# Kernel tuning notes

Measured on AMD Instinct MI355X. Metric: run time of the kernel, lower is better.

Reference implementation:

```python
import jax, jax.numpy as jnp
import numpy as np
from math import factorial

P = 3          # polynomial order
D_I = 4096     # sketch output dim per order
C = 512        # input channels
B, H, W = 8, 28, 28
GAMMA = 1e-4


def setup_inputs() -> dict:
    key = jax.random.key(0)
    k1, k2, k3 = jax.random.split(key, 3)
    x = jax.random.normal(k1, (B, H, W, C), dtype=jnp.float32)
    # AlphaInitializer: alpha_i = sqrt(exp(-2g) * (2g)^i / i!)
    gam2 = np.full(P + 1, 2.0 * GAMMA)
    numer = np.power(gam2, np.arange(P + 1))
    denom = np.array([factorial(i) for i in range(P + 1)], dtype=np.float64)
    alpha = jnp.asarray(np.sqrt(np.exp(-gam2) * numer / denom), dtype=jnp.float32)
    # count-sketch hash indices and sign bits, one pair per order t in [0, p)
    h_idx = jax.random.randint(k2, (P, C), 0, D_I)
    s_bits = jax.random.randint(k3, (P, C), 0, 2).astype(jnp.int32)
    return {"x": x, "alpha": alpha, "h_idx": h_idx, "s_bits": s_bits}


def reference(x, alpha, h_idx, s_bits):
    Bs, Hs, Ws, Ch = x.shape
    p = h_idx.shape[0]
    d_i = D_I
    signs = (2 * s_bits - 1).astype(x.dtype)          # (p, C) in {-1,+1}
    x_flat = x.reshape(-1, Ch)                        # (B*H*W, C)

    def count_sketch(h, s):
        # scatter-add channels into d_i buckets: equivalent to x_flat @ S
        return jnp.zeros((x_flat.shape[0], d_i), x.dtype).at[:, h].add(x_flat * s)

    sk = jax.vmap(count_sketch)(h_idx, signs)         # (p, N, d_i)
    xs = jnp.transpose(sk, (1, 0, 2)).reshape(Bs, Hs * Ws, p, d_i)

    xf = jnp.fft.fft(xs.astype(jnp.complex64), axis=-1)
    cp = jnp.cumprod(xf, axis=-2)[:, :, 1:, :]        # orders 2..p
    xi = jnp.real(jnp.fft.ifft(cp, axis=-1)).mean(axis=1)   # (B, p-1, d_i)

    x_p = xi * alpha[2:].reshape(1, p - 1, 1)
    zeroth = alpha[0] * jnp.ones((Bs, 1), x.dtype)
    first = alpha[1] * x.mean(axis=(1, 2))            # (B, C)
    phi = jnp.concatenate([zeroth, first, x_p.reshape(Bs, -1)], axis=-1)
    phi = jnp.sign(phi) * jnp.sqrt(jnp.abs(phi) + 1e-12)    # signed sqrt
    return phi / jnp.linalg.norm(phi, axis=-1, keepdims=True)
```

## Files before the change

### kernel.cpp

```cpp
#include <hip/hip_runtime.h>

#define BATCH 8
#define NPOS 784
#define CH 512
#define DI 4096
#define PPC 8
#define CHUNKS (NPOS / PPC)
#define PHI_LEN 8705
#define S_FLOATS (BATCH * 2 * 2049 * 2)
#define PHI_OFF S_FLOATS

__device__ __forceinline__ float2 cmul(float2 a, float2 b) {
  return make_float2(a.x * b.x - a.y * b.y, a.x * b.y + a.y * b.x);
}
__device__ __forceinline__ float2 f2add(float2 a, float2 b) {
  return make_float2(a.x + b.x, a.y + b.y);
}
__device__ __forceinline__ float2 f2sub(float2 a, float2 b) {
  return make_float2(a.x - b.x, a.y - b.y);
}

__device__ __forceinline__ void dft4(float2& a, float2& b, float2& c, float2& d) {
  float t0x = a.x + c.x, t0y = a.y + c.y;
  float t1x = a.x - c.x, t1y = a.y - c.y;
  float t2x = b.x + d.x, t2y = b.y + d.y;
  float t3x = b.x - d.x, t3y = b.y - d.y;
  a = make_float2(t0x + t2x, t0y + t2y);
  c = make_float2(t0x - t2x, t0y - t2y);
  b = make_float2(t1x + t3y, t1y - t3x);
  d = make_float2(t1x - t3y, t1y + t3x);
}

__device__ __forceinline__ void dft8(float2 v[8]) {
  float2 e0 = v[0], e1 = v[2], e2 = v[4], e3 = v[6];
  dft4(e0, e1, e2, e3);
  float2 o0 = v[1], o1 = v[3], o2 = v[5], o3 = v[7];
  dft4(o0, o1, o2, o3);
  const float r = 0.70710678118654752f;
  o1 = make_float2(r * (o1.x + o1.y), r * (o1.y - o1.x));
  o2 = make_float2(o2.y, -o2.x);
  o3 = make_float2(r * (o3.y - o3.x), -r * (o3.x + o3.y));
  v[0] = f2add(e0, o0); v[4] = f2sub(e0, o0);
  v[1] = f2add(e1, o1); v[5] = f2sub(e1, o1);
  v[2] = f2add(e2, o2); v[6] = f2sub(e2, o2);
  v[3] = f2add(e3, o3); v[7] = f2sub(e3, o3);
}

__device__ __forceinline__ void twiddle8(float2 v[8], float2 w) {
  float2 w2 = cmul(w, w);
  float2 w3 = cmul(w2, w);
  float2 w4 = cmul(w2, w2);
  v[1] = cmul(v[1], w);
  v[2] = cmul(v[2], w2);
  v[3] = cmul(v[3], w3);
  v[4] = cmul(v[4], w4);
  v[5] = cmul(v[5], cmul(w4, w));
  v[6] = cmul(v[6], cmul(w4, w2));
  v[7] = cmul(v[7], cmul(w4, w3));
}

__device__ __forceinline__ void fstage0(float2* Z, int t) {
  const int base = t << 3;
  const int mask0 = (t >> 1) & 15;
  float2 v[8];
  #pragma unroll
  for (int u = 0; u < 8; ++u) v[u] = Z[(base + u) ^ mask0];
  dft8(v);
  #pragma unroll
  for (int k = 0; k < 8; ++k) Z[(base + k) ^ mask0] = v[k];
}
__device__ __forceinline__ void fstage1(float2* Z, int t) {
  const int base = ((t >> 3) << 6) + (t & 7);
  const int g4 = (t >> 3) << 2;
  float sv_, cv_;
  __sincosf(-9.8174770424681038e-2f * (float)(t & 7), &sv_, &cv_);
  const float2 w1b = make_float2(cv_, sv_);
  float2 v[8];
  #pragma unroll
  for (int u = 0; u < 8; ++u)
    v[u] = Z[(base + (u << 3)) ^ ((g4 + (u >> 1)) & 15)];
  twiddle8(v, w1b);
  dft8(v);
  #pragma unroll
  for (int k = 0; k < 8; ++k)
    Z[(base + (k << 3)) ^ ((g4 + (k >> 1)) & 15)] = v[k];
}
__device__ __forceinline__ void fstage2(float2* Z, int t) {
  const int base = ((t >> 6) << 9) + (t & 63);
  const int jh = (t & 63) >> 4;
  float sv_, cv_;
  __sincosf(-1.2271846303085130e-2f * (float)(t & 63), &sv_, &cv_);
  const float2 w2b = make_float2(cv_, sv_);
  float2 v[8];
  #pragma unroll
  for (int u = 0; u < 8; ++u)
    v[u] = Z[(base + (u << 6)) ^ (((u << 2) + jh) & 15)];
  twiddle8(v, w2b);
  dft8(v);
  #pragma unroll
  for (int k = 0; k < 8; ++k)
    Z[(base + (k << 6)) ^ (((k << 2) + jh) & 15)] = v[k];
}
__device__ __forceinline__ void fstage3(float2* Z, int t) {
  const int mask3 = (t >> 4) & 15;
  float sv_, cv_;
  __sincosf(-1.5339807878856412e-3f * (float)t, &sv_, &cv_);
  const float2 w3b = make_float2(cv_, sv_);
  float2 v[8];
  #pragma unroll
  for (int u = 0; u < 8; ++u) v[u] = Z[(t + (u << 9)) ^ mask3];
  twiddle8(v, w3b);
  dft8(v);
  #pragma unroll
  for (int k = 0; k < 8; ++k) Z[(t + (k << 9)) ^ mask3] = v[k];
}

template <int MODE>
__device__ __forceinline__ void product_phase(
    float2* Z, int t, float2 carry[4], float2 acc2[4], float2 acc3[4],
    float& carryx, float& acc2x, float& acc3x) {
  const int mask3 = (t >> 4) & 15;
  #pragma unroll
  for (int jj = 0; jj < 4; ++jj) {
    const int k = t + (jj << 9);
    const int ak = k ^ mask3;
    const int m = (DI - k) & (DI - 1);
    const int am = m ^ ((m >> 4) & 15);
    float2 Zk = Z[ak], Zm = Z[am];
    Z[ak] = make_float2(0.f, 0.f);
    Z[am] = make_float2(0.f, 0.f);
    float2 E = make_float2(0.5f * (Zk.x + Zm.x), 0.5f * (Zk.y - Zm.y));
    float2 O = make_float2(0.5f * (Zk.y + Zm.y), -0.5f * (Zk.x - Zm.x));
    if (MODE == 0) {
      float2 P = cmul(E, O);
      carry[jj] = P;
      acc2[jj].x += P.x; acc2[jj].y += P.y;
    } else if (MODE == 1) {
      float2 P3 = cmul(carry[jj], E);
      acc3[jj].x += P3.x; acc3[jj].y += P3.y;
      carry[jj] = O;
    } else {
      float2 P = cmul(carry[jj], E);
      acc2[jj].x += P.x; acc2[jj].y += P.y;
      float2 P3 = cmul(P, O);
      acc3[jj].x += P3.x; acc3[jj].y += P3.y;
    }
  }
  if (t == 0) {
    float2 Zq = Z[2048];
    Z[2048] = make_float2(0.f, 0.f);
    if (MODE == 0) { carryx = Zq.x * Zq.y; acc2x += carryx; }
    else if (MODE == 1) { acc3x += carryx * Zq.x; carryx = Zq.y; }
    else { float tt = carryx * Zq.x; acc2x += tt; acc3x += tt * Zq.y; }
  }
}

__global__ __launch_bounds__(512) void cbp_stage1(
    const float* __restrict__ x, const float* __restrict__ alpha,
    const int* __restrict__ h_idx, const int* __restrict__ s_bits,
    float* __restrict__ ws) {
  __shared__ float2 ZA[DI];
  __shared__ float2 ZB[DI];
  float* ZAf = (float*)ZA;
  float* ZBf = (float*)ZB;
  const int t = threadIdx.x;
  const int bb = blockIdx.x / CHUNKS;
  const int ch = blockIdx.x % CHUNKS;

  auto mapq = [](int h, int s) {
    int r = ((h & 7) << 9) | (((h >> 3) & 7) << 6) | (((h >> 6) & 7) << 3) |
            (h >> 9);
    return (r ^ ((r >> 4) & 15)) | ((s ^ 1) << 31);
  };
  auto sgn = [](float v, int p) {
    return __int_as_float(__float_as_int(v) ^ ((unsigned)p & 0x80000000u));
  };
  const int q0 = mapq(h_idx[t], s_bits[t]);
  const int q1 = mapq(h_idx[CH + t], s_bits[CH + t]);
  const int q2 = mapq(h_idx[2 * CH + t], s_bits[2 * CH + t]);

  float2 acc2[4], acc3[4], carryA[4], carryB[4];
  #pragma unroll
  for (int j = 0; j < 4; ++j) {
    acc2[j] = make_float2(0.f, 0.f);
    acc3[j] = make_float2(0.f, 0.f);
  }
  float acc2x = 0.f, acc3x = 0.f, carryxA = 0.f, carryxB = 0.f;
  float xs = 0.f;

  #pragma unroll
  for (int q = 0; q < 8; ++q) {
    ZA[t + (q << 9)] = make_float2(0.f, 0.f);
    ZB[t + (q << 9)] = make_float2(0.f, 0.f);
  }
  __syncthreads();

  for (int ip = 0; ip < PPC / 4; ++ip) {
    const int n0 = bb * NPOS + ch * PPC + ip * 4;
    const float a0 = x[(size_t)n0 * CH + t];
    const float a1 = x[(size_t)(n0 + 1) * CH + t];
    const float b0 = x[(size_t)(n0 + 2) * CH + t];
    const float b1 = x[(size_t)(n0 + 3) * CH + t];
    xs += a0 + a1 + b0 + b1;

    atomicAdd(&ZAf[2 * (q0 & 0xFFF)], sgn(a0, q0));
    atomicAdd(&ZAf[2 * (q1 & 0xFFF) + 1], sgn(a0, q1));
    atomicAdd(&ZBf[2 * (q0 & 0xFFF)], sgn(b0, q0));
    atomicAdd(&ZBf[2 * (q1 & 0xFFF) + 1], sgn(b0, q1));
    __syncthreads();
    fstage0(ZA, t); fstage0(ZB, t); __syncthreads();
    fstage1(ZA, t); fstage1(ZB, t); __syncthreads();
    fstage2(ZA, t); fstage2(ZB, t); __syncthreads();
    fstage3(ZA, t); fstage3(ZB, t); __syncthreads();
    product_phase<0>(ZA, t, carryA, acc2, acc3, carryxA, acc2x, acc3x);
    product_phase<0>(ZB, t, carryB, acc2, acc3, carryxB, acc2x, acc3x);
    __syncthreads();

    atomicAdd(&ZAf[2 * (q2 & 0xFFF)], sgn(a0, q2));
    atomicAdd(&ZAf[2 * (q0 & 0xFFF) + 1], sgn(a1, q0));
    atomicAdd(&ZBf[2 * (q2 & 0xFFF)], sgn(b0, q2));
    atomicAdd(&ZBf[2 * (q0 & 0xFFF) + 1], sgn(b1, q0));
    __syncthreads();
    fstage0(ZA, t); fstage0(ZB, t); __syncthreads();
    fstage1(ZA, t); fstage1(ZB, t); __syncthreads();
    fstage2(ZA, t); fstage2(ZB, t); __syncthreads();
    fstage3(ZA, t); fstage3(ZB, t); __syncthreads();
    product_phase<1>(ZA, t, carryA, acc2, acc3, carryxA, acc2x, acc3x);
    product_phase<1>(ZB, t, carryB, acc2, acc3, carryxB, acc2x, acc3x);
    __syncthreads();

    atomicAdd(&ZAf[2 * (q1 & 0xFFF)], sgn(a1, q1));
    atomicAdd(&ZAf[2 * (q2 & 0xFFF) + 1], sgn(a1, q2));
    atomicAdd(&ZBf[2 * (q1 & 0xFFF)], sgn(b1, q1));
    atomicAdd(&ZBf[2 * (q2 & 0xFFF) + 1], sgn(b1, q2));
    __syncthreads();
    fstage0(ZA, t); fstage0(ZB, t); __syncthreads();
    fstage1(ZA, t); fstage1(ZB, t); __syncthreads();
    fstage2(ZA, t); fstage2(ZB, t); __syncthreads();
    fstage3(ZA, t); fstage3(ZB, t); __syncthreads();
    product_phase<2>(ZA, t, carryA, acc2, acc3, carryxA, acc2x, acc3x);
    product_phase<2>(ZB, t, carryB, acc2, acc3, carryxB, acc2x, acc3x);
    __syncthreads();
  }

  float* S = ws;
  #pragma unroll
  for (int jj = 0; jj < 4; ++jj) {
    const int k = t + (jj << 9);
    float* p2p = S + ((size_t)(bb * 2 + 0) * 2049 + k) * 2;
    atomicAdd(p2p, acc2[jj].x);
    atomicAdd(p2p + 1, acc2[jj].y);
    float* p3p = S + ((size_t)(bb * 2 + 1) * 2049 + k) * 2;
    atomicAdd(p3p, acc3[jj].x);
    atomicAdd(p3p + 1, acc3[jj].y);
  }
  if (t == 0) {
    atomicAdd(S + ((size_t)(bb * 2 + 0) * 2049 + 2048) * 2, acc2x);
    atomicAdd(S + ((size_t)(bb * 2 + 1) * 2049 + 2048) * 2, acc3x);
  }

  const float sc1 = alpha[1] * (1.0f / (float)NPOS);
  float* phi = ws + PHI_OFF;
  atomicAdd(&phi[(size_t)bb * PHI_LEN + 1 + t], xs * sc1);
}

__device__ inline void fft4096_r2(float2* Z, const float2* W, int tid) {
  for (int s = 1; s <= 12; ++s) {
    __syncthreads();
    const int half = 1 << (s - 1);
    const int tsh = 12 - s;
    #pragma unroll
    for (int q = 0; q < 8; ++q) {
      int bidx = tid + q * 256;
      int j = bidx & (half - 1);
      int i1 = ((bidx >> (s - 1)) << s) + j;
      int i2 = i1 + half;
      float2 w = W[j << tsh];
      float2 u = Z[i1];
      float2 v = Z[i2];
      float2 t = cmul(w, v);
      Z[i1] = make_float2(u.x + t.x, u.y + t.y);
      Z[i2] = make_float2(u.x - t.x, u.y - t.y);
    }
  }
  __syncthreads();
}

__global__ __launch_bounds__(256) void cbp_stage2(
    const float* __restrict__ ws_in, const float* __restrict__ alpha,
    float* __restrict__ ws_phi) {
  __shared__ float2 Z[DI];
  __shared__ float2 W[DI / 2];
  const int tid = threadIdx.x;

  for (int r = tid; r < DI / 2; r += 256) {
    float ang = 1.5339807878856412e-3f * (float)r;
    float sv, cv;
    sincosf(ang, &sv, &cv);
    W[r] = make_float2(cv, sv);
  }

  const int b = blockIdx.x >> 1;
  const int t = blockIdx.x & 1;
  const float* Sp = ws_in + (size_t)(b * 2 + t) * 2049 * 2;

  for (int k = tid; k <= 2048; k += 256) {
    float re = Sp[k * 2];
    float im = Sp[k * 2 + 1];
    Z[__brev((unsigned)k) >> 20] = make_float2(re, im);
    if (k > 0 && k < 2048) {
      Z[__brev((unsigned)(DI - k)) >> 20] = make_float2(re, -im);
    }
  }
  fft4096_r2(Z, W, tid);

  const float scale = alpha[2 + t] / ((float)DI * (float)NPOS);
  float* out = ws_phi + (size_t)b * PHI_LEN + 513 + t * DI;
  for (int d = tid; d < DI; d += 256) out[d] = Z[d].x * scale;
}

__global__ __launch_bounds__(256) void cbp_stage3(
    const float* __restrict__ ws_phi, const float* __restrict__ alpha,
    float* __restrict__ out) {
  __shared__ float red[4];
  const int b = blockIdx.x;
  const int tid = threadIdx.x;
  const float* pr = ws_phi + (size_t)b * PHI_LEN;
  const float a0 = alpha[0];

  float w[35];
  float ssum = 0.f;
  #pragma unroll
  for (int j = 0; j < 35; ++j) {
    const int idx = tid + j * 256;
    float wv = 0.f;
    if (idx < PHI_LEN) {
      float v = (idx == 0) ? a0 : pr[idx];
      float sq = sqrtf(fabsf(v) + 1e-12f);
      wv = (v > 0.f) ? sq : ((v < 0.f) ? -sq : 0.f);
    }
    w[j] = wv;
    ssum += wv * wv;
  }
  for (int off = 32; off > 0; off >>= 1) ssum += __shfl_down(ssum, off);
  if ((tid & 63) == 0) red[tid >> 6] = ssum;
  __syncthreads();
  const float tot = red[0] + red[1] + red[2] + red[3];
  const float inv = 1.0f / sqrtf(tot);

  #pragma unroll
  for (int j = 0; j < 35; ++j) {
    const int idx = tid + j * 256;
    if (idx < PHI_LEN) out[(size_t)b * PHI_LEN + idx] = w[j] * inv;
  }
}

extern "C" void kernel_launch(void* const* d_in, const int* in_sizes, int n_in,
                              void* d_out, int out_size, void* d_ws,
                              size_t ws_size, hipStream_t stream) {
  const float* x = (const float*)d_in[0];
  const float* alpha = (const float*)d_in[1];
  const int* h_idx = (const int*)d_in[2];
  const int* s_bits = (const int*)d_in[3];
  float* out = (float*)d_out;
  float* ws = (float*)d_ws;

  const size_t zero_bytes = (size_t)(S_FLOATS + BATCH * PHI_LEN) * sizeof(float);
  hipMemsetAsync(d_ws, 0, zero_bytes, stream);

  cbp_stage1<<<dim3(BATCH * CHUNKS), dim3(512), 0, stream>>>(x, alpha, h_idx,
                                                             s_bits, ws);
  cbp_stage2<<<dim3(BATCH * 2), dim3(256), 0, stream>>>(ws, alpha,
                                                        ws + PHI_OFF);
  cbp_stage3<<<dim3(BATCH), dim3(256), 0, stream>>>(ws + PHI_OFF, alpha, out);
}
```

Before: 241.7 us.

## Halve stage1 block to 256 threads with one FFT buffer and fused final stage

Reworks the sketch/FFT kernel to use 256 threads with a single 4096-point shared buffer. Each thread now handles two channels, loaded as a float2, and two butterfly groups per stage. The last radix-8 FFT stage is fused with the pointwise spectral product by pairing each thread's outputs with the mirror-index thread (512-t), which removes one barrier and one shared-memory round trip per FFT. Shared memory per block is halved to raise occupancy (launch_bounds 256,4), at the cost of more registers per thread and half as many positions processed concurrently per block.

```diff
diff --git a/kernel.cpp b/kernel.cpp
--- a/kernel.cpp
+++ b/kernel.cpp
@@ -59,113 +59,146 @@
   v[7] = cmul(v[7], cmul(w4, w3));
 }
 
-__device__ __forceinline__ void fstage0(float2* Z, int t) {
+__device__ __forceinline__ void s0pair(float2* Z, int t) {
   const int base = t << 3;
-  const int mask0 = (t >> 1) & 15;
-  float2 v[8];
-  #pragma unroll
-  for (int u = 0; u < 8; ++u) v[u] = Z[(base + u) ^ mask0];
-  dft8(v);
-  #pragma unroll
-  for (int k = 0; k < 8; ++k) Z[(base + k) ^ mask0] = v[k];
-}
-__device__ __forceinline__ void fstage1(float2* Z, int t) {
+  const int m0 = (t >> 1) & 15;
+  float2 a[8], b[8];
+  #pragma unroll
+  for (int u = 0; u < 8; ++u) a[u] = Z[(base + u) ^ m0];
+  #pragma unroll
+  for (int u = 0; u < 8; ++u) b[u] = Z[(2048 + base + u) ^ m0];
+  dft8(a);
+  #pragma unroll
+  for (int k = 0; k < 8; ++k) Z[(base + k) ^ m0] = a[k];
+  dft8(b);
+  #pragma unroll
+  for (int k = 0; k < 8; ++k) Z[(2048 + base + k) ^ m0] = b[k];
+}
+__device__ __forceinline__ void s1pair(float2* Z, int t) {
   const int base = ((t >> 3) << 6) + (t & 7);
   const int g4 = (t >> 3) << 2;
   float sv_, cv_;
   __sincosf(-9.8174770424681038e-2f * (float)(t & 7), &sv_, &cv_);
-  const float2 w1b = make_float2(cv_, sv_);
-  float2 v[8];
+  const float2 w = make_float2(cv_, sv_);
+  float2 a[8], b[8];
   #pragma unroll
   for (int u = 0; u < 8; ++u)
-    v[u] = Z[(base + (u << 3)) ^ ((g4 + (u >> 1)) & 15)];
-  twiddle8(v, w1b);
-  dft8(v);
+    a[u] = Z[(base + (u << 3)) ^ ((g4 + (u >> 1)) & 15)];
+  #pragma unroll
+  for (int u = 0; u < 8; ++u)
+    b[u] = Z[(2048 + base + (u << 3)) ^ ((g4 + (u >> 1)) & 15)];
+  twiddle8(a, w); dft8(a);
   #pragma unroll
   for (int k = 0; k < 8; ++k)
-    Z[(base + (k << 3)) ^ ((g4 + (k >> 1)) & 15)] = v[k];
-}
-__device__ __forceinline__ void fstage2(float2* Z, int t) {
+    Z[(base + (k << 3)) ^ ((g4 + (k >> 1)) & 15)] = a[k];
+  twiddle8(b, w); dft8(b);
+  #pragma unroll
+  for (int k = 0; k < 8; ++k)
+    Z[(2048 + base + (k << 3)) ^ ((g4 + (k >> 1)) & 15)] = b[k];
+}
+__device__ __forceinline__ void s2pair(float2* Z, int t) {
   const int base = ((t >> 6) << 9) + (t & 63);
   const int jh = (t & 63) >> 4;
   float sv_, cv_;
   __sincosf(-1.2271846303085130e-2f * (float)(t & 63), &sv_, &cv_);
-  const float2 w2b = make_float2(cv_, sv_);
-  float2 v[8];
+  const float2 w = make_float2(cv_, sv_);
+  float2 a[8], b[8];
   #pragma unroll
   for (int u = 0; u < 8; ++u)
-    v[u] = Z[(base + (u << 6)) ^ (((u << 2) + jh) & 15)];
-  twiddle8(v, w2b);
-  dft8(v);
+    a[u] = Z[(base + (u << 6)) ^ (((u << 2) + jh) & 15)];
+  #pragma unroll
+  for (int u = 0; u < 8; ++u)
+    b[u] = Z[(2048 + base + (u << 6)) ^ (((u << 2) + jh) & 15)];
+  twiddle8(a, w); dft8(a);
   #pragma unroll
   for (int k = 0; k < 8; ++k)
-    Z[(base + (k << 6)) ^ (((k << 2) + jh) & 15)] = v[k];
-}
-__device__ __forceinline__ void fstage3(float2* Z, int t) {
-  const int mask3 = (t >> 4) & 15;
+    Z[(base + (k << 6)) ^ (((k << 2) + jh) & 15)] = a[k];
+  twiddle8(b, w); dft8(b);
+  #pragma unroll
+  for (int k = 0; k < 8; ++k)
+    Z[(2048 + base + (k << 6)) ^ (((k << 2) + jh) & 15)] = b[k];
+}
+
+template <int MODE>
+__device__ __forceinline__ void prodpair(float2 Zk, float2 Zm, float2& carry,
+                                         float2& acc2, float2& acc3) {
+  float2 E = make_float2(0.5f * (Zk.x + Zm.x), 0.5f * (Zk.y - Zm.y));
+  float2 O = make_float2(0.5f * (Zk.y + Zm.y), -0.5f * (Zk.x - Zm.x));
+  if (MODE == 0) {
+    float2 P = cmul(E, O);
+    carry = P;
+    acc2.x += P.x; acc2.y += P.y;
+  } else if (MODE == 1) {
+    float2 P3 = cmul(carry, E);
+    acc3.x += P3.x; acc3.y += P3.y;
+    carry = O;
+  } else {
+    float2 P = cmul(carry, E);
+    acc2.x += P.x; acc2.y += P.y;
+    float2 P3 = cmul(P, O);
+    acc3.x += P3.x; acc3.y += P3.y;
+  }
+}
+template <int MODE>
+__device__ __forceinline__ void nyq(float2 Zq, float& carryx, float& acc2x,
+                                    float& acc3x) {
+  if (MODE == 0) { carryx = Zq.x * Zq.y; acc2x += carryx; }
+  else if (MODE == 1) { acc3x += carryx * Zq.x; carryx = Zq.y; }
+  else { float tt = carryx * Zq.x; acc2x += tt; acc3x += tt * Zq.y; }
+}
+
+template <int MODE>
+__device__ __forceinline__ void s3prod(float2* Z, int t, int bB,
+                                       float2 carry[8], float2 acc2[8],
+                                       float2 acc3[8], float& carryx,
+                                       float& acc2x, float& acc3x) {
+  const int mA = (t >> 4) & 15;
+  const int mB = (bB >> 4) & 15;
+  float2 a[8], b[8];
+  #pragma unroll
+  for (int u = 0; u < 8; ++u) a[u] = Z[(t + (u << 9)) ^ mA];
+  #pragma unroll
+  for (int u = 0; u < 8; ++u) b[u] = Z[(bB + (u << 9)) ^ mB];
+  #pragma unroll
+  for (int u = 0; u < 8; ++u) Z[(t + (u << 9)) ^ mA] = make_float2(0.f, 0.f);
+  #pragma unroll
+  for (int u = 0; u < 8; ++u) Z[(bB + (u << 9)) ^ mB] = make_float2(0.f, 0.f);
   float sv_, cv_;
   __sincosf(-1.5339807878856412e-3f * (float)t, &sv_, &cv_);
-  const float2 w3b = make_float2(cv_, sv_);
-  float2 v[8];
-  #pragma unroll
-  for (int u = 0; u < 8; ++u) v[u] = Z[(t + (u << 9)) ^ mask3];
-  twiddle8(v, w3b);
-  dft8(v);
-  #pragma unroll
-  for (int k = 0; k < 8; ++k) Z[(t + (k << 9)) ^ mask3] = v[k];
-}
-
-template <int MODE>
-__device__ __forceinline__ void product_phase(
-    float2* Z, int t, float2 carry[4], float2 acc2[4], float2 acc3[4],
-    float& carryx, float& acc2x, float& acc3x) {
-  const int mask3 = (t >> 4) & 15;
-  #pragma unroll
-  for (int jj = 0; jj < 4; ++jj) {
-    const int k = t + (jj << 9);
-    const int ak = k ^ mask3;
-    const int m = (DI - k) & (DI - 1);
-    const int am = m ^ ((m >> 4) & 15);
-    float2 Zk = Z[ak], Zm = Z[am];
-    Z[ak] = make_float2(0.f, 0.f);
-    Z[am] = make_float2(0.f, 0.f);
-    float2 E = make_float2(0.5f * (Zk.x + Zm.x), 0.5f * (Zk.y - Zm.y));
-    float2 O = make_float2(0.5f * (Zk.y + Zm.y), -0.5f * (Zk.x - Zm.x));
-    if (MODE == 0) {
-      float2 P = cmul(E, O);
-      carry[jj] = P;
-      acc2[jj].x += P.x; acc2[jj].y += P.y;
-    } else if (MODE == 1) {
-      float2 P3 = cmul(carry[jj], E);
-      acc3[jj].x += P3.x; acc3[jj].y += P3.y;
-      carry[jj] = O;
-    } else {
-      float2 P = cmul(carry[jj], E);
-      acc2[jj].x += P.x; acc2[jj].y += P.y;
-      float2 P3 = cmul(P, O);
-      acc3[jj].x += P3.x; acc3[jj].y += P3.y;
-    }
-  }
-  if (t == 0) {
-    float2 Zq = Z[2048];
-    Z[2048] = make_float2(0.f, 0.f);
-    if (MODE == 0) { carryx = Zq.x * Zq.y; acc2x += carryx; }
-    else if (MODE == 1) { acc3x += carryx * Zq.x; carryx = Zq.y; }
-    else { float tt = carryx * Zq.x; acc2x += tt; acc3x += tt * Zq.y; }
-  }
-}
-
-__global__ __launch_bounds__(512) void cbp_stage1(
+  twiddle8(a, make_float2(cv_, sv_));
+  dft8(a);
+  __sincosf(-1.5339807878856412e-3f * (float)bB, &sv_, &cv_);
+  twiddle8(b, make_float2(cv_, sv_));
+  dft8(b);
+  if (t != 0) {
+    #pragma unroll
+    for (int u = 0; u < 4; ++u)
+      prodpair<MODE>(a[u], b[7 - u], carry[u], acc2[u], acc3[u]);
+    #pragma unroll
+    for (int u = 0; u < 4; ++u)
+      prodpair<MODE>(b[u], a[7 - u], carry[4 + u], acc2[4 + u], acc3[4 + u]);
+  } else {
+    prodpair<MODE>(a[0], a[0], carry[0], acc2[0], acc3[0]);
+    prodpair<MODE>(a[1], a[7], carry[1], acc2[1], acc3[1]);
+    prodpair<MODE>(a[2], a[6], carry[2], acc2[2], acc3[2]);
+    prodpair<MODE>(a[3], a[5], carry[3], acc2[3], acc3[3]);
+    #pragma unroll
+    for (int u = 0; u < 4; ++u)
+      prodpair<MODE>(b[u], b[7 - u], carry[4 + u], acc2[4 + u], acc3[4 + u]);
+    nyq<MODE>(a[4], carryx, acc2x, acc3x);
+  }
+}
+
+__global__ __launch_bounds__(256, 4) void cbp_stage1(
     const float* __restrict__ x, const float* __restrict__ alpha,
     const int* __restrict__ h_idx, const int* __restrict__ s_bits,
     float* __restrict__ ws) {
-  __shared__ float2 ZA[DI];
-  __shared__ float2 ZB[DI];
-  float* ZAf = (float*)ZA;
-  float* ZBf = (float*)ZB;
+  __shared__ float2 Z[DI];
+  float* Zf = (float*)Z;
   const int t = threadIdx.x;
   const int bb = blockIdx.x / CHUNKS;
   const int ch = blockIdx.x % CHUNKS;
+  const int bB = (t == 0) ? 256 : (512 - t);
 
   auto mapq = [](int h, int s) {
     int r = ((h & 7) << 9) | (((h >> 3) & 7) << 6) | (((h >> 6) & 7) << 3) |
@@ -175,78 +208,72 @@
   auto sgn = [](float v, int p) {
     return __int_as_float(__float_as_int(v) ^ ((unsigned)p & 0x80000000u));
   };
-  const int q0 = mapq(h_idx[t], s_bits[t]);
-  const int q1 = mapq(h_idx[CH + t], s_bits[CH + t]);
-  const int q2 = mapq(h_idx[2 * CH + t], s_bits[2 * CH + t]);
-
-  float2 acc2[4], acc3[4], carryA[4], carryB[4];
-  #pragma unroll
-  for (int j = 0; j < 4; ++j) {
+  const int c0 = t * 2, c1 = c0 + 1;
+  const int q0a = mapq(h_idx[c0], s_bits[c0]);
+  const int q0b = mapq(h_idx[c1], s_bits[c1]);
+  const int q1a = mapq(h_idx[CH + c0], s_bits[CH + c0]);
+  const int q1b = mapq(h_idx[CH + c1], s_bits[CH + c1]);
+  const int q2a = mapq(h_idx[2 * CH + c0], s_bits[2 * CH + c0]);
+  const int q2b = mapq(h_idx[2 * CH + c1], s_bits[2 * CH + c1]);
+
+  float2 acc2[8], acc3[8], carry[8];
+  #pragma unroll
+  for (int j = 0; j < 8; ++j) {
     acc2[j] = make_float2(0.f, 0.f);
     acc3[j] = make_float2(0.f, 0.f);
   }
-  float acc2x = 0.f, acc3x = 0.f, carryxA = 0.f, carryxB = 0.f;
-  float xs = 0.f;
-
-  #pragma unroll
-  for (int q = 0; q < 8; ++q) {
-    ZA[t + (q << 9)] = make_float2(0.f, 0.f);
-    ZB[t + (q << 9)] = make_float2(0.f, 0.f);
-  }
+  float acc2x = 0.f, acc3x = 0.f, carryx = 0.f;
+  float xsa = 0.f, xsb = 0.f;
+
+  #pragma unroll
+  for (int q = 0; q < 16; ++q) Z[t + (q << 8)] = make_float2(0.f, 0.f);
   __syncthreads();
 
-  for (int ip = 0; ip < PPC / 4; ++ip) {
-    const int n0 = bb * NPOS + ch * PPC + ip * 4;
-    const float a0 = x[(size_t)n0 * CH + t];
-    const float a1 = x[(size_t)(n0 + 1) * CH + t];
-    const float b0 = x[(size_t)(n0 + 2) * CH + t];
-    const float b1 = x[(size_t)(n0 + 3) * CH + t];
-    xs += a0 + a1 + b0 + b1;
-
-    atomicAdd(&ZAf[2 * (q0 & 0xFFF)], sgn(a0, q0));
-    atomicAdd(&ZAf[2 * (q1 & 0xFFF) + 1], sgn(a0, q1));
-    atomicAdd(&ZBf[2 * (q0 & 0xFFF)], sgn(b0, q0));
-    atomicAdd(&ZBf[2 * (q1 & 0xFFF) + 1], sgn(b0, q1));
-    __syncthreads();
-    fstage0(ZA, t); fstage0(ZB, t); __syncthreads();
-    fstage1(ZA, t); fstage1(ZB, t); __syncthreads();
-    fstage2(ZA, t); fstage2(ZB, t); __syncthreads();
-    fstage3(ZA, t); fstage3(ZB, t); __syncthreads();
-    product_phase<0>(ZA, t, carryA, acc2, acc3, carryxA, acc2x, acc3x);
-    product_phase<0>(ZB, t, carryB, acc2, acc3, carryxB, acc2x, acc3x);
-    __syncthreads();
-
-    atomicAdd(&ZAf[2 * (q2 & 0xFFF)], sgn(a0, q2));
-    atomicAdd(&ZAf[2 * (q0 & 0xFFF) + 1], sgn(a1, q0));
-    atomicAdd(&ZBf[2 * (q2 & 0xFFF)], sgn(b0, q2));
-    atomicAdd(&ZBf[2 * (q0 & 0xFFF) + 1], sgn(b1, q0));
-    __syncthreads();
-    fstage0(ZA, t); fstage0(ZB, t); __syncthreads();
-    fstage1(ZA, t); fstage1(ZB, t); __syncthreads();
-    fstage2(ZA, t); fstage2(ZB, t); __syncthreads();
-    fstage3(ZA, t); fstage3(ZB, t); __syncthreads();
-    product_phase<1>(ZA, t, carryA, acc2, acc3, carryxA, acc2x, acc3x);
-    product_phase<1>(ZB, t, carryB, acc2, acc3, carryxB, acc2x, acc3x);
-    __syncthreads();
-
-    atomicAdd(&ZAf[2 * (q1 & 0xFFF)], sgn(a1, q1));
-    atomicAdd(&ZAf[2 * (q2 & 0xFFF) + 1], sgn(a1, q2));
-    atomicAdd(&ZBf[2 * (q1 & 0xFFF)], sgn(b1, q1));
-    atomicAdd(&ZBf[2 * (q2 & 0xFFF) + 1], sgn(b1, q2));
-    __syncthreads();
-    fstage0(ZA, t); fstage0(ZB, t); __syncthreads();
-    fstage1(ZA, t); fstage1(ZB, t); __syncthreads();
-    fstage2(ZA, t); fstage2(ZB, t); __syncthreads();
-    fstage3(ZA, t); fstage3(ZB, t); __syncthreads();
-    product_phase<2>(ZA, t, carryA, acc2, acc3, carryxA, acc2x, acc3x);
-    product_phase<2>(ZB, t, carryB, acc2, acc3, carryxB, acc2x, acc3x);
+  for (int ip = 0; ip < PPC / 2; ++ip) {
+    const int n0 = bb * NPOS + ch * PPC + ip * 2;
+    const float2 xv0 = *(const float2*)(x + (size_t)n0 * CH + c0);
+    const float2 xv1 = *(const float2*)(x + (size_t)(n0 + 1) * CH + c0);
+    xsa += xv0.x + xv1.x;
+    xsb += xv0.y + xv1.y;
+
+    atomicAdd(&Zf[2 * (q0a & 0xFFF)], sgn(xv0.x, q0a));
+    atomicAdd(&Zf[2 * (q0b & 0xFFF)], sgn(xv0.y, q0b));
+    atomicAdd(&Zf[2 * (q1a & 0xFFF) + 1], sgn(xv0.x, q1a));
+    atomicAdd(&Zf[2 * (q1b & 0xFFF) + 1], sgn(xv0.y, q1b));
+    __syncthreads();
+    s0pair(Z, t); __syncthreads();
+    s1pair(Z, t); __syncthreads();
+    s2pair(Z, t); __syncthreads();
+    s3prod<0>(Z, t, bB, carry, acc2, acc3, carryx, acc2x, acc3x);
+    __syncthreads();
+
+    atomicAdd(&Zf[2 * (q2a & 0xFFF)], sgn(xv0.x, q2a));
+    atomicAdd(&Zf[2 * (q2b & 0xFFF)], sgn(xv0.y, q2b));
+    atomicAdd(&Zf[2 * (q0a & 0xFFF) + 1], sgn(xv1.x, q0a));
+    atomicAdd(&Zf[2 * (q0b & 0xFFF) + 1], sgn(xv1.y, q0b));
+    __syncthreads();
+    s0pair(Z, t); __syncthreads();
+    s1pair(Z, t); __syncthreads();
+    s2pair(Z, t); __syncthreads();
+    s3prod<1>(Z, t, bB, carry, acc2, acc3, carryx, acc2x, acc3x);
+    __syncthreads();
+
+    atomicAdd(&Zf[2 * (q1a & 0xFFF)], sgn(xv1.x, q1a));
+    atomicAdd(&Zf[2 * (q1b & 0xFFF)], sgn(xv1.y, q1b));
+    atomicAdd(&Zf[2 * (q2a & 0xFFF) + 1], sgn(xv1.x, q2a));
+    atomicAdd(&Zf[2 * (q2b & 0xFFF) + 1], sgn(xv1.y, q2b));
+    __syncthreads();
+    s0pair(Z, t); __syncthreads();
+    s1pair(Z, t); __syncthreads();
+    s2pair(Z, t); __syncthreads();
+    s3prod<2>(Z, t, bB, carry, acc2, acc3, carryx, acc2x, acc3x);
     __syncthreads();
   }
 
   float* S = ws;
   #pragma unroll
-  for (int jj = 0; jj < 4; ++jj) {
-    const int k = t + (jj << 9);
+  for (int jj = 0; jj < 8; ++jj) {
+    const int k = (jj < 4) ? (t + (jj << 9)) : (bB + ((jj - 4) << 9));
     float* p2p = S + ((size_t)(bb * 2 + 0) * 2049 + k) * 2;
     atomicAdd(p2p, acc2[jj].x);
     atomicAdd(p2p + 1, acc2[jj].y);
@@ -261,7 +288,8 @@
 
   const float sc1 = alpha[1] * (1.0f / (float)NPOS);
   float* phi = ws + PHI_OFF;
-  atomicAdd(&phi[(size_t)bb * PHI_LEN + 1 + t], xs * sc1);
+  atomicAdd(&phi[(size_t)bb * PHI_LEN + 1 + c0], xsa * sc1);
+  atomicAdd(&phi[(size_t)bb * PHI_LEN + 1 + c1], xsb * sc1);
 }
 
 __device__ inline void fft4096_r2(float2* Z, const float2* W, int tid) {
@@ -368,7 +396,7 @@
   const size_t zero_bytes = (size_t)(S_FLOATS + BATCH * PHI_LEN) * sizeof(float);
   hipMemsetAsync(d_ws, 0, zero_bytes, stream);
 
-  cbp_stage1<<<dim3(BATCH * CHUNKS), dim3(512), 0, stream>>>(x, alpha, h_idx,
+  cbp_stage1<<<dim3(BATCH * CHUNKS), dim3(256), 0, stream>>>(x, alpha, h_idx,
                                                              s_bits, ws);
   cbp_stage2<<<dim3(BATCH * 2), dim3(256), 0, stream>>>(ws, alpha,
                                                         ws + PHI_OFF);
```

New measurement: 407.9 us. +68.8%, slower.
